# Optimization experiments

Hardware: AMD Instinct MI355X
Metric: run time of the kernel (lower is better)

Reference implementation:

```python
import jax, jax.numpy as jnp
import numpy as np

B, S, DM, H = 16, 4096, 512, 4
HD = DM // H  # head_dim = 128
EPS = 1e-5


def setup_inputs() -> dict:
    key = jax.random.key(0)
    ks = jax.random.split(key, 9)
    sc = 1.0 / np.sqrt(DM)
    inp = {
        "x": jax.random.normal(ks[0], (B, S, DM), dtype=jnp.float32),
        "Wq_w": jax.random.normal(ks[1], (DM, DM), dtype=jnp.float32) * sc,
        "Wq_b": jnp.zeros((DM,), dtype=jnp.float32),
        "Wk_w": jax.random.normal(ks[2], (DM, DM), dtype=jnp.float32) * sc,
        "Wk_b": jnp.zeros((DM,), dtype=jnp.float32),
        "Wv_w": jax.random.normal(ks[3], (DM, DM), dtype=jnp.float32) * sc,
        "Wv_b": jnp.zeros((DM,), dtype=jnp.float32),
        "Wo_w": jax.random.normal(ks[4], (DM, DM), dtype=jnp.float32) * sc,
        "Wo_b": jnp.zeros((DM,), dtype=jnp.float32),
        "ln_g": jnp.ones((DM,), dtype=jnp.float32),
        "ln_b": jnp.zeros((DM,), dtype=jnp.float32),
    }
    return inp


def _forward(x, Wq_w, Wq_b, Wk_w, Wk_b, Wv_w, Wv_b, Wo_w, Wo_b, ln_g, ln_b):
    b, s, _ = x.shape
    # Linear projections, viewed as [B,S,H,HD] exactly as the torch code does
    Q = (x @ Wq_w.T + Wq_b).reshape(b, s, H, HD)
    K = (x @ Wk_w.T + Wk_b).reshape(b, s, H, HD)
    V = (x @ Wv_w.T + Wv_b).reshape(b, s, H, HD)
    # NOTE: source never permutes heads to dim 1, so attention is over the
    # HEAD axis per token: scores [B,S,H,H]
    scores = jnp.einsum("bshd,bstd->bsht", Q, K) / np.sqrt(HD).astype(np.float32)
    attn = jax.nn.softmax(scores, axis=-1)  # dropout is identity in eval
    out = jnp.einsum("bsht,bstd->bshd", attn, V).reshape(b, s, DM)
    out = out @ Wo_w.T + Wo_b
    y = out + x  # input_dim == output_dim -> residual branch taken
    mu = jnp.mean(y, axis=-1, keepdims=True)
    var = jnp.mean((y - mu) ** 2, axis=-1, keepdims=True)
    return (y - mu) * jax.lax.rsqrt(var + EPS) * ln_g + ln_b


def reference(x, Wq_w, Wq_b, Wk_w, Wk_b, Wv_w, Wv_b, Wo_w, Wo_b, ln_g, ln_b):
    return _forward(x, Wq_w, Wq_b, Wk_w, Wk_b, Wv_w, Wv_b, Wo_w, Wo_b, ln_g, ln_b)
```

## Files before the change

### kernel.cpp

```cpp
#include <hip/hip_runtime.h>
#include <stdint.h>

#define NTOK 65536
#define DMODEL 512
#define QKVN 1536
#define LN_EPS 1e-5f

typedef __attribute__((ext_vector_type(8))) short short8;
typedef __attribute__((ext_vector_type(8))) unsigned short ushort8;
typedef __attribute__((ext_vector_type(4))) float float4_t;

static __device__ __forceinline__ float bf2f(unsigned short u) {
    union { unsigned int i; float f; } c; c.i = ((unsigned int)u) << 16; return c.f;
}
static __device__ __forceinline__ unsigned short f2bf(float f) {
    union { float f; unsigned int i; } c; c.f = f;
    unsigned int x = c.i;
    return (unsigned short)((x + 0x7fffu + ((x >> 16) & 1u)) >> 16);
}
static __device__ __forceinline__ void gload_lds16(const void* g, void* l) {
    __builtin_amdgcn_global_load_lds((const __attribute__((address_space(1))) void*)g,
                                     (__attribute__((address_space(3))) void*)l, 16, 0, 0);
}

#define BAR() __builtin_amdgcn_s_barrier()
#define WAITL0() asm volatile("s_waitcnt lgkmcnt(0)" ::: "memory")
#define WVM(n) asm volatile("s_waitcnt vmcnt(" #n ")" ::: "memory")
#define MFMA(a, b, c) __builtin_amdgcn_mfma_f32_16x16x32_bf16((a), (b), (c), 0, 0, 0)

__global__ __launch_bounds__(256) void cast_x_kernel(const float* __restrict__ x,
                                                     unsigned short* __restrict__ xb, int n8) {
    int stride = gridDim.x * blockDim.x;
    for (int i = blockIdx.x * blockDim.x + threadIdx.x; i < n8; i += stride) {
        const float4_t* p = (const float4_t*)(x + (size_t)i * 8);
        float4_t a = p[0], b = p[1];
        ushort8 v;
        v[0] = f2bf(a[0]); v[1] = f2bf(a[1]); v[2] = f2bf(a[2]); v[3] = f2bf(a[3]);
        v[4] = f2bf(b[0]); v[5] = f2bf(b[1]); v[6] = f2bf(b[2]); v[7] = f2bf(b[3]);
        *(ushort8*)(xb + (size_t)i * 8) = v;
    }
}

__global__ __launch_bounds__(256) void prep_w_kernel(
    const float* __restrict__ wq, const float* __restrict__ wk, const float* __restrict__ wv,
    const float* __restrict__ wo,
    const float* __restrict__ bq, const float* __restrict__ bk, const float* __restrict__ bv,
    unsigned short* __restrict__ wqkv, unsigned short* __restrict__ wpack,
    float* __restrict__ bias_qkv) {
    const int WN = DMODEL * DMODEL;
    int tid = blockIdx.x * blockDim.x + threadIdx.x;
    int stride = gridDim.x * blockDim.x;
    for (int j = tid; j < 3 * WN; j += stride) {
        int seg = j / WN, idx = j - seg * WN;
        const float* src = (seg == 0) ? wq : (seg == 1) ? wk : wv;
        wqkv[j] = f2bf(src[idx]);
    }
    for (int j = tid; j < WN; j += stride) {
        int e = j & 7, l = (j >> 3) & 63, nf = (j >> 9) & 31, kt = j >> 14;
        int row = nf * 16 + (l & 15);
        int k = kt * 32 + ((l >> 4) << 3) + e;
        wpack[j] = f2bf(wo[row * 512 + k]);
    }
    for (int j = tid; j < QKVN; j += stride)
        bias_qkv[j] = (j < 512) ? bq[j] : (j < 1024) ? bk[j - 512] : bv[j - 1024];
}

__global__ __launch_bounds__(512, 2) void gemm1_kernel(
    const unsigned short* __restrict__ A, const unsigned short* __restrict__ Bw,
    const float* __restrict__ bias, unsigned short* __restrict__ Cout) {
    __shared__ unsigned short As[4][256 * 32];
    __shared__ unsigned short Bs[4][256 * 32];

    const int b = blockIdx.x;
    const int L = (b & 7) * 192 + (b >> 3);
    const int bm = L / 6;
    const int bn = L - bm * 6;

    const int t = threadIdx.x;
    const int lane = t & 63;
    const int w = t >> 6;
    const int wm = w >> 2, wn = w & 3;

    const unsigned short* Ab = A + (size_t)bm * 256 * 512;
    const unsigned short* Bb = Bw + (size_t)bn * 256 * 512;

    const int i0 = t, i1 = 512 + t;
    const int r0 = i0 >> 2, s0 = (i0 & 3) ^ ((r0 >> 1) & 3);
    const int r1 = i1 >> 2, s1 = (i1 & 3) ^ ((r1 >> 1) & 3);

#define STAGE_A1(kt) do { \
        gload_lds16(Ab + r0 * 512 + (kt) * 32 + s0 * 8, &As[(kt) & 3][i0 * 8]); \
        gload_lds16(Ab + r1 * 512 + (kt) * 32 + s1 * 8, &As[(kt) & 3][i1 * 8]); } while (0)
#define STAGE_B1(kt) do { \
        gload_lds16(Bb + r0 * 512 + (kt) * 32 + s0 * 8, &Bs[(kt) & 3][i0 * 8]); \
        gload_lds16(Bb + r1 * 512 + (kt) * 32 + s1 * 8, &Bs[(kt) & 3][i1 * 8]); } while (0)

    int aoff[8], boff[4];
#pragma unroll
    for (int m = 0; m < 8; m++) {
        int row = wm * 128 + m * 16 + (lane & 15);
        aoff[m] = row * 32 + (((lane >> 4) ^ ((row >> 1) & 3)) * 8);
    }
#pragma unroll
    for (int n = 0; n < 4; n++) {
        int row = wn * 64 + n * 16 + (lane & 15);
        boff[n] = row * 32 + (((lane >> 4) ^ ((row >> 1) & 3)) * 8);
    }

    float4_t acc[8][4];
#pragma unroll
    for (int m = 0; m < 8; m++)
#pragma unroll
        for (int n = 0; n < 4; n++) acc[m][n] = (float4_t){0.f, 0.f, 0.f, 0.f};

    STAGE_A1(0); STAGE_B1(0);
    STAGE_A1(1); STAGE_B1(1);
    STAGE_A1(2); STAGE_B1(2);
    WVM(8);
    BAR();

    short8 ar[8], br[4];
#pragma unroll
    for (int kt = 0; kt < 16; ++kt) {
        const int sl = kt & 3;
#pragma unroll
        for (int m = 0; m < 8; m++) ar[m] = *(const short8*)&As[sl][aoff[m]];
        br[0] = *(const short8*)&Bs[sl][boff[0]];
        br[1] = *(const short8*)&Bs[sl][boff[1]];
        if (kt <= 12) STAGE_A1(kt + 3);
        BAR();
        WAITL0();
        __builtin_amdgcn_s_setprio(1);
#pragma unroll
        for (int m = 0; m < 8; m++) {
            acc[m][0] = MFMA(ar[m], br[0], acc[m][0]);
            acc[m][1] = MFMA(ar[m], br[1], acc[m][1]);
        }
        __builtin_amdgcn_s_setprio(0);
        BAR();
        br[2] = *(const short8*)&Bs[sl][boff[2]];
        br[3] = *(const short8*)&Bs[sl][boff[3]];
        if (kt <= 12) STAGE_B1(kt + 3);
        BAR();
        WAITL0();
        __builtin_amdgcn_s_setprio(1);
#pragma unroll
        for (int m = 0; m < 8; m++) {
            acc[m][2] = MFMA(ar[m], br[2], acc[m][2]);
            acc[m][3] = MFMA(ar[m], br[3], acc[m][3]);
        }
        __builtin_amdgcn_s_setprio(0);
        if (kt <= 12) { WVM(8); }
        else if (kt == 13) { WVM(4); }
        else if (kt == 14) { WVM(0); }
        BAR();
    }

    const int orow0 = bm * 256 + wm * 128;
    const int ocol0 = bn * 256 + wn * 64;
#pragma unroll
    for (int m = 0; m < 8; m++) {
#pragma unroll
        for (int n = 0; n < 4; n++) {
            int col = ocol0 + n * 16 + (lane & 15);
            float bv = bias[col];
#pragma unroll
            for (int j = 0; j < 4; j++) {
                int row = orow0 + m * 16 + (lane >> 4) * 4 + j;
                Cout[(size_t)row * QKVN + col] = f2bf(acc[m][n][j] + bv);
            }
        }
    }
#undef STAGE_A1
#undef STAGE_B1
}

__global__ __launch_bounds__(256, 3) void attn_o_ln_kernel(
    const unsigned short* __restrict__ qkv, const unsigned short* __restrict__ Wpack,
    const float* __restrict__ bo, const float* __restrict__ xres,
    const float* __restrict__ lng, const float* __restrict__ lnb,
    float* __restrict__ Y) {
    __shared__ __align__(16) unsigned char AOs[32 * 1024];
    __shared__ float red[4][32][2];

    const int blk = blockIdx.x;
    const int T0 = blk * 32;
    const int t = threadIdx.x;
    const int lane = t & 63;
    const int w = t >> 6;
    const int g = lane >> 4;
    const int sl = lane & 15;

    const float scale = 0.08838834764831845f;

#pragma unroll
    for (int r = 0; r < 2; ++r) {
        const int tr = w * 8 + r * 4 + g;
        const unsigned short* base = qkv + (size_t)(T0 + tr) * QKVN + sl * 8;

        short8 qr[4], kr[4], vr[4];
#pragma unroll
        for (int h = 0; h < 4; h++) {
            qr[h] = *(const short8*)(base + h * 128);
            kr[h] = *(const short8*)(base + 512 + h * 128);
            vr[h] = *(const short8*)(base + 1024 + h * 128);
        }
        float qf[4][8];
#pragma unroll
        for (int h = 0; h < 4; h++)
#pragma unroll
            for (int d = 0; d < 8; d++) qf[h][d] = bf2f((unsigned short)qr[h][d]);

        float s[4][4];
#pragma unroll
        for (int h = 0; h < 4; h++)
#pragma unroll
            for (int tt = 0; tt < 4; tt++) s[h][tt] = 0.f;
#pragma unroll
        for (int tt = 0; tt < 4; tt++) {
            float kf[8];
#pragma unroll
            for (int d = 0; d < 8; d++) kf[d] = bf2f((unsigned short)kr[tt][d]);
#pragma unroll
            for (int h = 0; h < 4; h++)
#pragma unroll
                for (int d = 0; d < 8; d++) s[h][tt] += qf[h][d] * kf[d];
        }
#pragma unroll
        for (int mask = 1; mask < 16; mask <<= 1) {
#pragma unroll
            for (int h = 0; h < 4; h++)
#pragma unroll
                for (int tt = 0; tt < 4; tt++)
                    s[h][tt] += __shfl_xor(s[h][tt], mask, 64);
        }
        float p[4][4];
#pragma unroll
        for (int h = 0; h < 4; h++) {
            float m0 = fmaxf(fmaxf(s[h][0], s[h][1]), fmaxf(s[h][2], s[h][3])) * scale;
            float sum = 0.f;
#pragma unroll
            for (int tt = 0; tt < 4; tt++) { p[h][tt] = __expf(s[h][tt] * scale - m0); sum += p[h][tt]; }
            float rr = __frcp_rn(sum);
#pragma unroll
            for (int tt = 0; tt < 4; tt++) p[h][tt] *= rr;
        }
        float o[4][8];
#pragma unroll
        for (int h = 0; h < 4; h++)
#pragma unroll
            for (int d = 0; d < 8; d++) o[h][d] = 0.f;
#pragma unroll
        for (int tt = 0; tt < 4; tt++) {
            float vf[8];
#pragma unroll
            for (int d = 0; d < 8; d++) vf[d] = bf2f((unsigned short)vr[tt][d]);
#pragma unroll
            for (int h = 0; h < 4; h++) {
                float ph = p[h][tt];
#pragma unroll
                for (int d = 0; d < 8; d++) o[h][d] += ph * vf[d];
            }
        }
#pragma unroll
        for (int h = 0; h < 4; h++) {
            ushort8 pk;
#pragma unroll
            for (int d = 0; d < 8; d++) pk[d] = f2bf(o[h][d]);
            int off = tr * 1024 + ((h * 256 + sl * 16) ^ ((tr & 7) << 4));
            *(ushort8*)(AOs + off) = pk;
        }
    }
    __syncthreads();

    const unsigned short* Bbase = Wpack + ((size_t)(w * 8) * 64 + lane) * 8;

    float4_t acc[2][8];
#pragma unroll
    for (int m = 0; m < 2; m++)
#pragma unroll
        for (int n = 0; n < 8; n++) acc[m][n] = (float4_t){0.f, 0.f, 0.f, 0.f};

    const int arow0 = (lane & 15);
    const int arow1 = 16 + (lane & 15);

    short8 bnext[8];
#pragma unroll
    for (int n = 0; n < 8; n++) bnext[n] = *(const short8*)(Bbase + n * 512);

#pragma unroll
    for (int kt = 0; kt < 16; ++kt) {
        short8 bcur[8];
#pragma unroll
        for (int n = 0; n < 8; n++) bcur[n] = bnext[n];
        if (kt < 15) {
#pragma unroll
            for (int n = 0; n < 8; n++)
                bnext[n] = *(const short8*)(Bbase + (size_t)(kt + 1) * 16384 + n * 512);
        }
        int lslot = kt * 64 + (lane >> 4) * 16;
        short8 a0 = *(const short8*)(AOs + arow0 * 1024 + (lslot ^ ((arow0 & 7) << 4)));
        short8 a1 = *(const short8*)(AOs + arow1 * 1024 + (lslot ^ ((arow1 & 7) << 4)));
#pragma unroll
        for (int n = 0; n < 8; n++) {
            acc[0][n] = MFMA(a0, bcur[n], acc[0][n]);
            acc[1][n] = MFMA(a1, bcur[n], acc[1][n]);
        }
    }

    float bias8[8], gc8[8], bc8[8];
#pragma unroll
    for (int n = 0; n < 8; n++) {
        int c = w * 128 + n * 16 + (lane & 15);
        bias8[n] = bo[c]; gc8[n] = lng[c]; bc8[n] = lnb[c];
    }
#pragma unroll
    for (int m = 0; m < 2; m++) {
#pragma unroll
        for (int j = 0; j < 4; j++) {
            int grow = T0 + m * 16 + (lane >> 4) * 4 + j;
            const float* xr = xres + (size_t)grow * 512;
#pragma unroll
            for (int n = 0; n < 8; n++) {
                int c = w * 128 + n * 16 + (lane & 15);
                acc[m][n][j] += bias8[n] + xr[c];
            }
        }
    }
#pragma unroll
    for (int m = 0; m < 2; m++) {
#pragma unroll
        for (int j = 0; j < 4; j++) {
            float s = 0.f, s2 = 0.f;
#pragma unroll
            for (int n = 0; n < 8; n++) { float v = acc[m][n][j]; s += v; s2 += v * v; }
#pragma unroll
            for (int mask = 1; mask < 16; mask <<= 1) {
                s += __shfl_xor(s, mask, 64);
                s2 += __shfl_xor(s2, mask, 64);
            }
            if ((lane & 15) == 0) {
                int rl = m * 16 + (lane >> 4) * 4 + j;
                red[w][rl][0] = s;
                red[w][rl][1] = s2;
            }
        }
    }
    __syncthreads();
#pragma unroll
    for (int m = 0; m < 2; m++) {
#pragma unroll
        for (int j = 0; j < 4; j++) {
            int rl = m * 16 + (lane >> 4) * 4 + j;
            float s = red[0][rl][0] + red[1][rl][0] + red[2][rl][0] + red[3][rl][0];
            float s2 = red[0][rl][1] + red[1][rl][1] + red[2][rl][1] + red[3][rl][1];
            float mu = s * (1.f / 512.f);
            float var = s2 * (1.f / 512.f) - mu * mu;
            float inv = rsqrtf(var + LN_EPS);
            int grow = T0 + rl;
            float* yp = Y + (size_t)grow * 512;
#pragma unroll
            for (int n = 0; n < 8; n++) {
                int c = w * 128 + n * 16 + (lane & 15);
                yp[c] = (acc[m][n][j] - mu) * inv * gc8[n] + bc8[n];
            }
        }
    }
}

extern "C" void kernel_launch(void* const* d_in, const int* in_sizes, int n_in,
                              void* d_out, int out_size, void* d_ws, size_t ws_size,
                              hipStream_t stream) {
    const float* x   = (const float*)d_in[0];
    const float* wq  = (const float*)d_in[1];
    const float* bq  = (const float*)d_in[2];
    const float* wk  = (const float*)d_in[3];
    const float* bk  = (const float*)d_in[4];
    const float* wv  = (const float*)d_in[5];
    const float* bv  = (const float*)d_in[6];
    const float* wo  = (const float*)d_in[7];
    const float* bo  = (const float*)d_in[8];
    const float* lng = (const float*)d_in[9];
    const float* lnb = (const float*)d_in[10];

    char* ws = (char*)d_ws;
    unsigned short* Xb    = (unsigned short*)(ws);
    unsigned short* Wqkv  = (unsigned short*)(ws + 67108864);
    unsigned short* Wpack = (unsigned short*)(ws + 68681728);
    float*          Bqkv  = (float*)        (ws + 69206016);
    unsigned short* QKV   = (unsigned short*)(ws + 69212160);
    float* Y = (float*)d_out;

    cast_x_kernel<<<2048, 256, 0, stream>>>(x, Xb, NTOK * 512 / 8);
    prep_w_kernel<<<1024, 256, 0, stream>>>(wq, wk, wv, wo, bq, bk, bv, Wqkv, Wpack, Bqkv);

    gemm1_kernel<<<(NTOK / 256) * (QKVN / 256), 512, 0, stream>>>(Xb, Wqkv, Bqkv, QKV);

    attn_o_ln_kernel<<<NTOK / 32, 256, 0, stream>>>(QKV, Wpack, bo, x, lng, lnb, Y);
}
```

Baseline: 338.1 us.

## Raise attn_o_ln occupancy by trimming registers and reusing LDS for reductions

Raises the launch-bounds wave target from 3 to 4 blocks per CU and reduces register pressure so that fits. The head-attention loop and the K loop are no longer unrolled, and B-fragment prefetch double-buffering is dropped. The LayerNorm reduction scratch now aliases the AO LDS buffer, with an added barrier. bf16 packing uses the hardware v_cvt_pk_bf16_f32 instruction. The trade-off is less latency hiding within a wave (no prefetch, no unroll) in exchange for more waves per CU.

```diff
diff --git a/kernel.cpp b/kernel.cpp
--- a/kernel.cpp
+++ b/kernel.cpp
@@ -9,6 +9,7 @@
 typedef __attribute__((ext_vector_type(8))) short short8;
 typedef __attribute__((ext_vector_type(8))) unsigned short ushort8;
 typedef __attribute__((ext_vector_type(4))) float float4_t;
+typedef __attribute__((ext_vector_type(4))) unsigned int uint4_t;
 
 static __device__ __forceinline__ float bf2f(unsigned short u) {
     union { unsigned int i; float f; } c; c.i = ((unsigned int)u) << 16; return c.f;
@@ -17,6 +18,11 @@
     union { float f; unsigned int i; } c; c.f = f;
     unsigned int x = c.i;
     return (unsigned short)((x + 0x7fffu + ((x >> 16) & 1u)) >> 16);
+}
+static __device__ __forceinline__ unsigned int cvt_pk_bf16(float lo, float hi) {
+    unsigned int r;
+    asm("v_cvt_pk_bf16_f32 %0, %1, %2" : "=v"(r) : "v"(lo), "v"(hi));
+    return r;
 }
 static __device__ __forceinline__ void gload_lds16(const void* g, void* l) {
     __builtin_amdgcn_global_load_lds((const __attribute__((address_space(1))) void*)g,
@@ -175,13 +181,13 @@
 #undef STAGE_B1
 }
 
-__global__ __launch_bounds__(256, 3) void attn_o_ln_kernel(
+__global__ __launch_bounds__(256, 4) void attn_o_ln_kernel(
     const unsigned short* __restrict__ qkv, const unsigned short* __restrict__ Wpack,
     const float* __restrict__ bo, const float* __restrict__ xres,
     const float* __restrict__ lng, const float* __restrict__ lnb,
     float* __restrict__ Y) {
     __shared__ __align__(16) unsigned char AOs[32 * 1024];
-    __shared__ float red[4][32][2];
+    float* red = (float*)AOs;
 
     const int blk = blockIdx.x;
     const int T0 = blk * 32;
@@ -193,7 +199,7 @@
 
     const float scale = 0.08838834764831845f;
 
-#pragma unroll
+#pragma unroll 1
     for (int r = 0; r < 2; ++r) {
         const int tr = w * 8 + r * 4 + g;
         const unsigned short* base = qkv + (size_t)(T0 + tr) * QKVN + sl * 8;
@@ -264,16 +270,20 @@
         }
 #pragma unroll
         for (int h = 0; h < 4; h++) {
-            ushort8 pk;
-#pragma unroll
-            for (int d = 0; d < 8; d++) pk[d] = f2bf(o[h][d]);
+            uint4_t pk;
+            pk[0] = cvt_pk_bf16(o[h][0], o[h][1]);
+            pk[1] = cvt_pk_bf16(o[h][2], o[h][3]);
+            pk[2] = cvt_pk_bf16(o[h][4], o[h][5]);
+            pk[3] = cvt_pk_bf16(o[h][6], o[h][7]);
             int off = tr * 1024 + ((h * 256 + sl * 16) ^ ((tr & 7) << 4));
-            *(ushort8*)(AOs + off) = pk;
+            *(uint4_t*)(AOs + off) = pk;
         }
     }
     __syncthreads();
 
-    const unsigned short* Bbase = Wpack + ((size_t)(w * 8) * 64 + lane) * 8;
+    const unsigned short* Bb2 = Wpack + ((size_t)(w * 8) * 64 + lane) * 8;
+    const int arow0 = sl;
+    const int arow1 = 16 + sl;
 
     float4_t acc[2][8];
 #pragma unroll
@@ -281,32 +291,22 @@
 #pragma unroll
         for (int n = 0; n < 8; n++) acc[m][n] = (float4_t){0.f, 0.f, 0.f, 0.f};
 
-    const int arow0 = (lane & 15);
-    const int arow1 = 16 + (lane & 15);
-
-    short8 bnext[8];
-#pragma unroll
-    for (int n = 0; n < 8; n++) bnext[n] = *(const short8*)(Bbase + n * 512);
-
-#pragma unroll
+#pragma unroll 1
     for (int kt = 0; kt < 16; ++kt) {
-        short8 bcur[8];
-#pragma unroll
-        for (int n = 0; n < 8; n++) bcur[n] = bnext[n];
-        if (kt < 15) {
-#pragma unroll
-            for (int n = 0; n < 8; n++)
-                bnext[n] = *(const short8*)(Bbase + (size_t)(kt + 1) * 16384 + n * 512);
-        }
+        short8 bfr[8];
+#pragma unroll
+        for (int n = 0; n < 8; n++)
+            bfr[n] = *(const short8*)(Bb2 + (size_t)kt * 16384 + n * 512);
         int lslot = kt * 64 + (lane >> 4) * 16;
         short8 a0 = *(const short8*)(AOs + arow0 * 1024 + (lslot ^ ((arow0 & 7) << 4)));
         short8 a1 = *(const short8*)(AOs + arow1 * 1024 + (lslot ^ ((arow1 & 7) << 4)));
 #pragma unroll
         for (int n = 0; n < 8; n++) {
-            acc[0][n] = MFMA(a0, bcur[n], acc[0][n]);
-            acc[1][n] = MFMA(a1, bcur[n], acc[1][n]);
-        }
-    }
+            acc[0][n] = MFMA(a0, bfr[n], acc[0][n]);
+            acc[1][n] = MFMA(a1, bfr[n], acc[1][n]);
+        }
+    }
+    __syncthreads();
 
     float bias8[8], gc8[8], bc8[8];
 #pragma unroll
@@ -341,8 +341,8 @@
             }
             if ((lane & 15) == 0) {
                 int rl = m * 16 + (lane >> 4) * 4 + j;
-                red[w][rl][0] = s;
-                red[w][rl][1] = s2;
+                red[(w * 32 + rl) * 2 + 0] = s;
+                red[(w * 32 + rl) * 2 + 1] = s2;
             }
         }
     }
@@ -352,8 +352,12 @@
 #pragma unroll
         for (int j = 0; j < 4; j++) {
             int rl = m * 16 + (lane >> 4) * 4 + j;
-            float s = red[0][rl][0] + red[1][rl][0] + red[2][rl][0] + red[3][rl][0];
-            float s2 = red[0][rl][1] + red[1][rl][1] + red[2][rl][1] + red[3][rl][1];
+            float s = 0.f, s2 = 0.f;
+#pragma unroll
+            for (int i = 0; i < 4; i++) {
+                s += red[(i * 32 + rl) * 2 + 0];
+                s2 += red[(i * 32 + rl) * 2 + 1];
+            }
             float mu = s * (1.f / 512.f);
             float var = s2 * (1.f / 512.f) - mu * mu;
             float inv = rsqrtf(var + LN_EPS);
```

Measured after the change: 410.4 us. 21.4% more time.
